# Kernel tuning notes

Measured on AMD Instinct MI355X. Metric: run time of the kernel, lower is better.

Reference implementation:

```python
import jax, jax.numpy as jnp
import numpy as np


def setup_inputs() -> dict:
    key = jax.random.key(0)
    ks = jax.random.split(key, 8)
    N, T, D, H = 2048, 365, 16, 64
    s = lambda d: 1.0 / np.sqrt(d)
    return {
        "x": jax.random.normal(ks[0], (N, T, D), dtype=jnp.float32),
        "A": jax.random.uniform(ks[1], (N, N), dtype=jnp.float32) * (1.0 / N),
        "W_ih": jax.random.normal(ks[2], (D, 4 * H), dtype=jnp.float32) * s(D),
        "W_hh": jax.random.normal(ks[3], (H, 4 * H), dtype=jnp.float32) * s(H),
        "bias": jnp.zeros((4 * H,), dtype=jnp.float32),
        "W_q": jax.random.normal(ks[4], (H, H), dtype=jnp.float32) * s(H),
        "b_q": jnp.zeros((H,), dtype=jnp.float32),
        "W_dense": jax.random.normal(ks[5], (H, 1), dtype=jnp.float32) * s(H),
        "b_dense": jnp.zeros((1,), dtype=jnp.float32),
    }


def reference(x, A, W_ih, W_hh, bias, W_q, b_q, W_dense, b_dense):
    N, T, D = x.shape
    H = W_hh.shape[0]

    def step(carry, x_t):
        h, c = carry
        gates = x_t @ W_ih + h @ W_hh + bias  # [N, 4H]
        i_t = jax.nn.sigmoid(gates[:, :H])
        f_t = jax.nn.sigmoid(gates[:, H:2 * H])
        g_t = jnp.tanh(gates[:, 2 * H:3 * H])
        o_t = jax.nn.sigmoid(gates[:, 3 * H:])
        q_t = jnp.tanh(h @ W_q + b_q)          # [N, H]
        c = f_t * (c + A @ q_t) + i_t * g_t    # graph-conv injected into cell state
        h = o_t * jnp.tanh(c)
        return (h, c), h

    h0 = jnp.zeros((N, H), dtype=x.dtype)
    c0 = jnp.zeros((N, H), dtype=x.dtype)
    # scan over time: x -> [T, N, D]
    _, hs = jax.lax.scan(step, (h0, c0), jnp.swapaxes(x, 0, 1))
    hidden_seq = jnp.swapaxes(hs, 0, 1)        # [N, T, H]
    out = hidden_seq @ W_dense + b_dense       # [N, T, 1]
    return out
```

## Files before the change

kernel.cpp:

```cpp
#include <hip/hip_runtime.h>
#include <stdint.h>

#define NN 2048
#define TT 365
#define DD 16
#define HH 64
#define NBLK 128
#define NTHR 1024
#define SMEM_BYTES 150016
#define QSLOT_U32 65536
#define SENT32 0xFFFFFFFFu

typedef __attribute__((ext_vector_type(8))) short bf16x8;
typedef __attribute__((ext_vector_type(4))) float f32x4;
typedef __attribute__((ext_vector_type(4))) unsigned int u32x4;

__device__ __forceinline__ unsigned short f2bf(float f) {
  union { float f; uint32_t u; } z; z.f = f;
  uint32_t r = z.u + 0x7fffu + ((z.u >> 16) & 1u);
  return (unsigned short)(r >> 16);
}
__device__ __forceinline__ float sigmoid_(float x) { return 1.f / (1.f + __expf(-x)); }
__device__ __forceinline__ float tanh_(float x) {
  float ax = fabsf(x);
  float e = __expf(-2.f * ax);
  float r = (1.f - e) / (1.f + e);
  return x < 0.f ? -r : r;
}
__device__ __forceinline__ bf16x8 asbf(u32x4 v) { return __builtin_bit_cast(bf16x8, v); }

__global__ __launch_bounds__(NTHR) __attribute__((amdgpu_waves_per_eu(4, 4)))
void rgcn_persist(
    const float* __restrict__ X, const float* __restrict__ Af,
    const float* __restrict__ Wih, const float* __restrict__ Whh,
    const float* __restrict__ Bias, const float* __restrict__ Wq,
    const float* __restrict__ Bq, const float* __restrict__ Wd,
    const float* __restrict__ Bd, float* __restrict__ Out,
    uint32_t* qRing, uint32_t* flags, int rdepth, int ringfull)
{
  extern __shared__ __align__(16) char smem[];
  unsigned short* afrag = (unsigned short*)smem;
  unsigned short* whxT  = (unsigned short*)(smem + 65536);
  unsigned short* wqT   = (unsigned short*)(smem + 118784);
  float*          sh_g  = (float*)(smem + 128000);
  f32x4*          sh_part = (f32x4*)(smem + 128000);
  unsigned short* sh_hx = (unsigned short*)(smem + 144640);
  unsigned int*   cnt   = (unsigned int*)(smem + 147968);

  const int tid = threadIdx.x;
  const int w = tid >> 6;
  const int c = tid & 63;
  const int base = blockIdx.x * 16;
  const int m = c & 15, quad = c >> 4;
  const int nt = w & 3, kh = w >> 2;

  for (int i = tid; i < 256 * 104; i += NTHR) {
    int n = i / 104, k = i - n * 104;
    float v = (k < 64) ? Whh[k * 256 + n] : (k < 80) ? Wih[(k - 64) * 256 + n] : 0.f;
    whxT[i] = f2bf(v);
  }
  for (int i = tid; i < 64 * 72; i += NTHR) {
    int n = i / 72, k = i - n * 72;
    wqT[i] = (k < 64) ? f2bf(Wq[k * 64 + n]) : (unsigned short)0;
  }
  for (int i = tid; i < 16 * NN; i += NTHR) {
    int r = i >> 11, k = i & (NN - 1);
    afrag[(k >> 5) * 512 + (((k >> 3) & 3) * 16 + r) * 8 + (k & 7)] =
        f2bf(Af[(size_t)(base + r) * NN + k]);
  }
  for (int i = tid; i < 16 * 104; i += NTHR) sh_hx[i] = 0;
  __syncthreads();
  if (c < 16) sh_hx[w * 104 + 64 + c] = f2bf(X[(size_t)(base + w) * (TT * DD) + c]);
  if (tid == 0) *cnt = 0u;
  __syncthreads();

  const float b_i = Bias[c], b_f = Bias[64 + c], b_g = Bias[128 + c], b_o = Bias[192 + c];
  const float wdc = Wd[c], bdc = Bd[0];
  const float bqv = (w < 4) ? Bq[w * 16 + m] : 0.f;
  const unsigned short* afp = afrag + (kh * 16) * 512 + c * 8;

  float creg = 0.f, hreg = 0.f;
  float o0 = 0.f, o1 = 0.f, o2 = 0.f, o3 = 0.f, o4 = 0.f, o5 = 0.f;
  float px = 0.f;

  const uint32_t qoff = (uint32_t)((kh * 32 + (quad >> 1)) * 2048 +
                                   (nt * 16 + m) * 32 + (quad & 1) * 16);
  const uint32_t poff = (uint32_t)(blockIdx.x * 2048 + (w * 16 + m) * 32 + quad * 8);

  if (w < 4) {
    unsigned short qb = f2bf(tanh_(bqv));
    uint32_t pp = (uint32_t)qb | ((uint32_t)qb << 16);
    unsigned long long v = (unsigned long long)pp | ((unsigned long long)pp << 32);
    unsigned long long* dst = (unsigned long long*)((char*)qRing + poff);
    __hip_atomic_store(dst, v, __ATOMIC_RELAXED, __HIP_MEMORY_SCOPE_AGENT);
    if (!ringfull) {
      asm volatile("s_waitcnt vmcnt(0)" ::: "memory");
      if (c == 0) {
        unsigned old = atomicAdd(cnt, 1u);
        if (old == 3u)
          __hip_atomic_store(&flags[blockIdx.x * 16], 1u,
                             __ATOMIC_RELAXED, __HIP_MEMORY_SCOPE_AGENT);
      }
    }
  }

  int slotR = 0;
  for (int t = 0; t < TT; ++t) {
    const int slotW = (slotR + 1 == rdepth) ? 0 : slotR + 1;

    if (((t & 1) == 0) && c < 32) {
      int tt = t + 1 + (c >> 4);
      px = (tt < TT) ? X[(size_t)(base + w) * (TT * DD) + tt * DD + (c & 15)] : 0.f;
    }

    f32x4 dg = {0.f, 0.f, 0.f, 0.f};
    {
      const unsigned short* ar = sh_hx + m * 104 + quad * 8;
      const unsigned short* br = whxT + (w * 16 + m) * 104 + quad * 8;
      #pragma unroll
      for (int ch = 0; ch < 3; ++ch)
        dg = __builtin_amdgcn_mfma_f32_16x16x32_bf16(*(const bf16x8*)(ar + ch * 32),
                                                     *(const bf16x8*)(br + ch * 32), dg, 0, 0, 0);
    }
    #pragma unroll
    for (int r = 0; r < 4; ++r)
      sh_g[(quad * 4 + r) * 260 + w * 16 + m] = dg[r];
    __syncthreads();

    float gi = sigmoid_(b_i + sh_g[w * 260 + c]);
    float gf = sigmoid_(b_f + sh_g[w * 260 + 64 + c]);
    float gg = tanh_  (b_g + sh_g[w * 260 + 128 + c]);
    float go = sigmoid_(b_o + sh_g[w * 260 + 192 + c]);
    __syncthreads();

    const uint64_t qa =
        (uint64_t)((char*)qRing + (size_t)slotR * (QSLOT_U32 * 4) + qoff);
    u32x4 qv[16];
    if (ringfull) {
      unsigned pend = 0xFFFFu;
      int pass = 0;
      do {
        if (pass) __builtin_amdgcn_s_sleep(1);
        #pragma unroll
        for (int ch = 0; ch < 16; ++ch)
          if (pend & (1u << ch))
            asm volatile("global_load_dwordx4 %0, %1, off sc0 sc1"
                         : "=v"(qv[ch]) : "v"(qa + (uint64_t)(ch * 4096)) : "memory");
        asm volatile("s_waitcnt vmcnt(0)" ::: "memory");
        __builtin_amdgcn_sched_barrier(0);
        #pragma unroll
        for (int ch = 0; ch < 16; ++ch)
          if (pend & (1u << ch))
            if (qv[ch][0] != SENT32 && qv[ch][2] != SENT32)
              pend &= ~(1u << ch);
        pass = 1;
      } while (!__all(pend == 0));
    } else {
      const uint32_t target = (uint32_t)(t + 1);
      const int src = 32 * kh + (c & 31);
      for (;;) {
        uint32_t f = __hip_atomic_load(&flags[src * 16],
                                       __ATOMIC_RELAXED, __HIP_MEMORY_SCOPE_AGENT);
        if (__all((int)(f >= target))) break;
        __builtin_amdgcn_s_sleep(1);
      }
      __builtin_amdgcn_fence(__ATOMIC_ACQUIRE, "agent");
      #pragma unroll
      for (int ch = 0; ch < 16; ++ch)
        qv[ch] = *(const u32x4*)(qa + (uint64_t)(ch * 4096));
    }

    f32x4 acc0 = {0.f,0.f,0.f,0.f}, acc1 = {0.f,0.f,0.f,0.f};
    #pragma unroll
    for (int ch = 0; ch < 16; ch += 2) {
      acc0 = __builtin_amdgcn_mfma_f32_16x16x32_bf16(
          *(const bf16x8*)(afp + ch * 512), asbf(qv[ch]), acc0, 0, 0, 0);
      acc1 = __builtin_amdgcn_mfma_f32_16x16x32_bf16(
          *(const bf16x8*)(afp + (ch + 1) * 512), asbf(qv[ch + 1]), acc1, 0, 0, 0);
    }
    sh_part[w * 65 + c] = acc0 + acc1;
    __syncthreads();

    f32x4 vs;
    {
      const f32x4* sp = sh_part;
      const int li = (w >> 2) * 16 + m;
      f32x4 p0 = sp[(0 * 4 + quad) * 65 + li];
      f32x4 p1 = sp[(1 * 4 + quad) * 65 + li];
      f32x4 p2 = sp[(2 * 4 + quad) * 65 + li];
      f32x4 p3 = sp[(3 * 4 + quad) * 65 + li];
      vs = (p0 + p1) + (p2 + p3);
    }
    float a01 = (w & 1) ? vs[1] : vs[0];
    float a23 = (w & 1) ? vs[3] : vs[2];
    float aqv = (w & 2) ? a23 : a01;

    creg = gf * (creg + aqv) + gi * gg;
    hreg = go * tanh_(creg);
    sh_hx[w * 104 + c] = f2bf(hreg);
    {
      float xw = (t & 1) ? __shfl(px, (c & 15) + 16) : px;
      if (c < 16) sh_hx[w * 104 + 64 + c] = f2bf(xw);
    }
    __syncthreads();

    if (w < 4 && t < TT - 1) {
      f32x4 dq = {0.f, 0.f, 0.f, 0.f};
      const unsigned short* ar = sh_hx + m * 104 + quad * 8;
      const unsigned short* br = wqT + (w * 16 + m) * 72 + quad * 8;
      #pragma unroll
      for (int k2 = 0; k2 < 2; ++k2)
        dq = __builtin_amdgcn_mfma_f32_16x16x32_bf16(*(const bf16x8*)(ar + k2 * 32),
                                                     *(const bf16x8*)(br + k2 * 32), dq, 0, 0, 0);
      unsigned short b0 = f2bf(tanh_(dq[0] + bqv));
      unsigned short b1 = f2bf(tanh_(dq[1] + bqv));
      unsigned short b2 = f2bf(tanh_(dq[2] + bqv));
      unsigned short b3 = f2bf(tanh_(dq[3] + bqv));
      unsigned long long v =
          (unsigned long long)((uint32_t)b0 | ((uint32_t)b1 << 16)) |
          ((unsigned long long)((uint32_t)b2 | ((uint32_t)b3 << 16)) << 32);
      unsigned long long* dst = (unsigned long long*)
          ((char*)qRing + (size_t)slotW * (QSLOT_U32 * 4) + poff);
      __hip_atomic_store(dst, v, __ATOMIC_RELAXED, __HIP_MEMORY_SCOPE_AGENT);
      if (!ringfull) {
        asm volatile("s_waitcnt vmcnt(0)" ::: "memory");
        if (c == 0) {
          unsigned old = atomicAdd(cnt, 1u);
          if (old == (unsigned)(4 * t + 7))
            __hip_atomic_store(&flags[blockIdx.x * 16], (uint32_t)(t + 2),
                               __ATOMIC_RELAXED, __HIP_MEMORY_SCOPE_AGENT);
        }
      }
    }

    {
      float red = hreg * wdc;
      #pragma unroll
      for (int off = 32; off; off >>= 1) red += __shfl_xor(red, off);
      float ov = red + bdc;
      switch (t >> 6) {
        case 0: if (c == (t & 63)) o0 = ov; break;
        case 1: if (c == (t & 63)) o1 = ov; break;
        case 2: if (c == (t & 63)) o2 = ov; break;
        case 3: if (c == (t & 63)) o3 = ov; break;
        case 4: if (c == (t & 63)) o4 = ov; break;
        default: if (c == (t & 63)) o5 = ov; break;
      }
    }

    slotR = slotW;
  }

  {
    float* orow = Out + (size_t)(base + w) * TT;
    orow[c] = o0;
    orow[64 + c] = o1;
    orow[128 + c] = o2;
    orow[192 + c] = o3;
    orow[256 + c] = o4;
    if (320 + c < TT) orow[320 + c] = o5;
  }
}

extern "C" void kernel_launch(void* const* d_in, const int* in_sizes, int n_in,
                              void* d_out, int out_size, void* d_ws, size_t ws_size,
                              hipStream_t stream) {
  const float* X    = (const float*)d_in[0];
  const float* Af   = (const float*)d_in[1];
  const float* Wih  = (const float*)d_in[2];
  const float* Whh  = (const float*)d_in[3];
  const float* Bias = (const float*)d_in[4];
  const float* Wq   = (const float*)d_in[5];
  const float* Bq   = (const float*)d_in[6];
  const float* Wd   = (const float*)d_in[7];
  const float* Bd   = (const float*)d_in[8];
  float* Out = (float*)d_out;

  char* ws = (char*)d_ws;
  uint32_t* flags = (uint32_t*)ws;
  uint32_t* qRing = (uint32_t*)(ws + 8192);

  long long avail = (long long)ws_size - 8192;
  int rdepth = (int)(avail / (QSLOT_U32 * 4));
  if (rdepth > TT + 1) rdepth = TT + 1;
  if (rdepth < 2) rdepth = 2;
  int ringfull = (rdepth >= TT + 1) ? 1 : 0;

  hipFuncSetAttribute((const void*)rgcn_persist,
                      hipFuncAttributeMaxDynamicSharedMemorySize, SMEM_BYTES);
  hipMemsetAsync(ws, 0, 8192, stream);
  if (ringfull)
    hipMemsetAsync(qRing, 0xFF, (size_t)rdepth * QSLOT_U32 * 4, stream);
  hipLaunchKernelGGL(rgcn_persist, dim3(NBLK), dim3(NTHR), SMEM_BYTES, stream,
                     X, Af, Wih, Whh, Bias, Wq, Bq, Wd, Bd, Out, qRing, flags,
                     rdepth, ringfull);
}
```

Baseline: 2.185 ms.

## Replace sentinel-polling ring with per-block flag barrier polled by one wave

Drops the sentinel-based full-ring path, where every wave spun on 16 q-ring loads checking for 0xFFFFFFFF. Every block now publishes a per-block step flag, and wave 0 polls all 128 flags before a block barrier, after which all waves do plain q loads. This also removes the 0xFF memset of the whole ring, and the flag publish is moved after the output reduction so its vmcnt wait overlaps other work. The trade-off is a wait for all 128 producer blocks instead of only the needed chunks, with one wave polling for the whole block. In the full-ring path there is no acquire fence after the wait, so memory ordering relies on the plain loads.

```diff
diff --git a/kernel.cpp b/kernel.cpp
--- a/kernel.cpp
+++ b/kernel.cpp
@@ -9,7 +9,6 @@
 #define NTHR 1024
 #define SMEM_BYTES 150016
 #define QSLOT_U32 65536
-#define SENT32 0xFFFFFFFFu
 
 typedef __attribute__((ext_vector_type(8))) short bf16x8;
 typedef __attribute__((ext_vector_type(4))) float f32x4;
@@ -93,14 +92,12 @@
     unsigned long long v = (unsigned long long)pp | ((unsigned long long)pp << 32);
     unsigned long long* dst = (unsigned long long*)((char*)qRing + poff);
     __hip_atomic_store(dst, v, __ATOMIC_RELAXED, __HIP_MEMORY_SCOPE_AGENT);
-    if (!ringfull) {
-      asm volatile("s_waitcnt vmcnt(0)" ::: "memory");
-      if (c == 0) {
-        unsigned old = atomicAdd(cnt, 1u);
-        if (old == 3u)
-          __hip_atomic_store(&flags[blockIdx.x * 16], 1u,
-                             __ATOMIC_RELAXED, __HIP_MEMORY_SCOPE_AGENT);
-      }
+    asm volatile("s_waitcnt vmcnt(0)" ::: "memory");
+    if (c == 0) {
+      unsigned old = atomicAdd(cnt, 1u);
+      if (old == 3u)
+        __hip_atomic_store(&flags[blockIdx.x * 16], 1u,
+                           __ATOMIC_RELAXED, __HIP_MEMORY_SCOPE_AGENT);
     }
   }
 
@@ -131,44 +128,28 @@
     float gf = sigmoid_(b_f + sh_g[w * 260 + 64 + c]);
     float gg = tanh_  (b_g + sh_g[w * 260 + 128 + c]);
     float go = sigmoid_(b_o + sh_g[w * 260 + 192 + c]);
-    __syncthreads();
+
+    if (w == 0) {
+      const uint32_t target = (uint32_t)(t + 1);
+      for (;;) {
+        uint32_t f0 = __hip_atomic_load(&flags[c * 16],
+                                        __ATOMIC_RELAXED, __HIP_MEMORY_SCOPE_AGENT);
+        uint32_t f1 = __hip_atomic_load(&flags[(64 + c) * 16],
+                                        __ATOMIC_RELAXED, __HIP_MEMORY_SCOPE_AGENT);
+        if (__all((f0 >= target) && (f1 >= target))) break;
+        __builtin_amdgcn_s_sleep(1);
+      }
+    }
+    __syncthreads();
+    if (!ringfull)
+      __builtin_amdgcn_fence(__ATOMIC_ACQUIRE, "agent");
 
     const uint64_t qa =
         (uint64_t)((char*)qRing + (size_t)slotR * (QSLOT_U32 * 4) + qoff);
     u32x4 qv[16];
-    if (ringfull) {
-      unsigned pend = 0xFFFFu;
-      int pass = 0;
-      do {
-        if (pass) __builtin_amdgcn_s_sleep(1);
-        #pragma unroll
-        for (int ch = 0; ch < 16; ++ch)
-          if (pend & (1u << ch))
-            asm volatile("global_load_dwordx4 %0, %1, off sc0 sc1"
-                         : "=v"(qv[ch]) : "v"(qa + (uint64_t)(ch * 4096)) : "memory");
-        asm volatile("s_waitcnt vmcnt(0)" ::: "memory");
-        __builtin_amdgcn_sched_barrier(0);
-        #pragma unroll
-        for (int ch = 0; ch < 16; ++ch)
-          if (pend & (1u << ch))
-            if (qv[ch][0] != SENT32 && qv[ch][2] != SENT32)
-              pend &= ~(1u << ch);
-        pass = 1;
-      } while (!__all(pend == 0));
-    } else {
-      const uint32_t target = (uint32_t)(t + 1);
-      const int src = 32 * kh + (c & 31);
-      for (;;) {
-        uint32_t f = __hip_atomic_load(&flags[src * 16],
-                                       __ATOMIC_RELAXED, __HIP_MEMORY_SCOPE_AGENT);
-        if (__all((int)(f >= target))) break;
-        __builtin_amdgcn_s_sleep(1);
-      }
-      __builtin_amdgcn_fence(__ATOMIC_ACQUIRE, "agent");
-      #pragma unroll
-      for (int ch = 0; ch < 16; ++ch)
-        qv[ch] = *(const u32x4*)(qa + (uint64_t)(ch * 4096));
-    }
+    #pragma unroll
+    for (int ch = 0; ch < 16; ++ch)
+      qv[ch] = *(const u32x4*)(qa + (uint64_t)(ch * 4096));
 
     f32x4 acc0 = {0.f,0.f,0.f,0.f}, acc1 = {0.f,0.f,0.f,0.f};
     #pragma unroll
@@ -222,15 +203,6 @@
       unsigned long long* dst = (unsigned long long*)
           ((char*)qRing + (size_t)slotW * (QSLOT_U32 * 4) + poff);
       __hip_atomic_store(dst, v, __ATOMIC_RELAXED, __HIP_MEMORY_SCOPE_AGENT);
-      if (!ringfull) {
-        asm volatile("s_waitcnt vmcnt(0)" ::: "memory");
-        if (c == 0) {
-          unsigned old = atomicAdd(cnt, 1u);
-          if (old == (unsigned)(4 * t + 7))
-            __hip_atomic_store(&flags[blockIdx.x * 16], (uint32_t)(t + 2),
-                               __ATOMIC_RELAXED, __HIP_MEMORY_SCOPE_AGENT);
-        }
-      }
     }
 
     {
@@ -245,6 +217,16 @@
         case 3: if (c == (t & 63)) o3 = ov; break;
         case 4: if (c == (t & 63)) o4 = ov; break;
         default: if (c == (t & 63)) o5 = ov; break;
+      }
+    }
+
+    if (w < 4 && t < TT - 1) {
+      asm volatile("s_waitcnt vmcnt(0)" ::: "memory");
+      if (c == 0) {
+        unsigned old = atomicAdd(cnt, 1u);
+        if (old == (unsigned)(4 * t + 7))
+          __hip_atomic_store(&flags[blockIdx.x * 16], (uint32_t)(t + 2),
+                             __ATOMIC_RELAXED, __HIP_MEMORY_SCOPE_AGENT);
       }
     }
 
@@ -289,8 +271,6 @@
   hipFuncSetAttribute((const void*)rgcn_persist,
                       hipFuncAttributeMaxDynamicSharedMemorySize, SMEM_BYTES);
   hipMemsetAsync(ws, 0, 8192, stream);
-  if (ringfull)
-    hipMemsetAsync(qRing, 0xFF, (size_t)rdepth * QSLOT_U32 * 4, stream);
   hipLaunchKernelGGL(rgcn_persist, dim3(NBLK), dim3(NTHR), SMEM_BYTES, stream,
                      X, Af, Wih, Whh, Bias, Wq, Bq, Wd, Bd, Out, qRing, flags,
                      rdepth, ringfull);
```

Measured after the change: 2.026 ms. -7.3%, faster.
